# Performance work log

Measured on AMD Instinct MI355X. Metric: run time of the kernel, lower is better.

The kernel has to match this reference:

```python
import jax, jax.numpy as jnp
import numpy as np
from jax import lax

S = 1024   # max_num_segments
CB = 25    # color_hist_bins
TB = 10    # texture_hist_bins
EPS = 1e-12


def setup_inputs() -> dict:
    key = jax.random.key(0)
    k1, k2, k3, k4 = jax.random.split(key, 4)
    B, C, R, H, W = 8, 3, 8, 512, 512
    img = jax.random.normal(k1, (B, C, H, W), jnp.float32)
    imgs_bins = jax.random.randint(k2, (B, C, H, W), 0, CB, jnp.int32)
    grads_bins = jax.random.randint(k3, (B, C, R, H, W), 0, TB, jnp.int32)
    reg_lab = jax.random.randint(k4, (B, H, W), 0, S, jnp.int32)
    return {"img": img, "imgs_bins": imgs_bins, "grads_bins": grads_bins, "reg_lab": reg_lab}


def reference(img, imgs_bins, grads_bins, reg_lab):
    B, C, H, W = img.shape
    R = grads_bins.shape[2]
    HW = H * W
    lab = reg_lab.astype(jnp.int32)

    # ---- area_per_segment: scatter_add of ones over flattened labels ----
    flat = (lab.reshape(B, HW) + (jnp.arange(B, dtype=jnp.int32) * S)[:, None]).reshape(-1)
    area = jnp.zeros(B * S, jnp.int32).at[flat].add(1).reshape(B, S)

    # ---- bbox_per_segment: scatter amin/amax of pixel coordinates ----
    yy, xx = jnp.meshgrid(jnp.arange(H, dtype=jnp.int32),
                          jnp.arange(W, dtype=jnp.int32), indexing='ij')
    xb = jnp.broadcast_to(xx.reshape(HW), (B, HW)).reshape(-1)
    yb = jnp.broadcast_to(yy.reshape(HW), (B, HW)).reshape(-1)
    xmin = jnp.full(B * S, W, jnp.int32).at[flat].min(xb)
    ymin = jnp.full(B * S, H, jnp.int32).at[flat].min(yb)
    xmax = jnp.zeros(B * S, jnp.int32).at[flat].max(xb)
    ymax = jnp.zeros(B * S, jnp.int32).at[flat].max(yb)
    # torch does xywh[2:] -= xywh[:2] (no +1), so w = xmax - xmin
    bbox_xywh = jnp.stack([xmin, ymin, xmax - xmin, ymax - ymin], -1).reshape(B, S, 4)

    area_f = area.astype(jnp.float32)

    # ---- color histogram: scatter_add of ones into [B,C,S*CB] ----
    ci = (lab[:, None, :, :] * CB + imgs_bins).reshape(B * C, HW)
    ci = (ci + (jnp.arange(B * C, dtype=jnp.int32) * (S * CB))[:, None]).reshape(-1)
    color_hist = jnp.zeros(B * C * S * CB, jnp.float32).at[ci].add(1.0).reshape(B, C, S, CB)
    color_hist = color_hist.transpose(0, 2, 1, 3).reshape(B, S, C * CB)  # [B,S,C*CB]
    color_hist = color_hist / (area_f * float(C) + EPS)[..., None]

    # ---- texture histogram: scatter_add of ones into [B,C,R,S*TB] ----
    ti = (lab[:, None, None, :, :] * TB + grads_bins).reshape(B * C * R, HW)
    ti = (ti + (jnp.arange(B * C * R, dtype=jnp.int32) * (S * TB))[:, None]).reshape(-1)
    texture_hist = jnp.zeros(B * C * R * S * TB, jnp.float32).at[ti].add(1.0).reshape(B, C, R, S, TB)
    texture_hist = texture_hist.transpose(0, 3, 1, 2, 4).reshape(B, S, C * R * TB)  # [B,S,C*R*TB]
    texture_hist = texture_hist / (area_f * float(C * R) + EPS)[..., None]

    # ---- image_scharr_gradients: depthwise-style conv2d, padding=1 ----
    sx = jnp.array([[-3., 0., 3.], [-10., 0., 10.], [-3., 0., 3.]], jnp.float32)
    kern = jnp.stack([sx, sx.T])[:, None]  # [2,1,3,3]
    grads = lax.conv_general_dilated(img.reshape(B * C, 1, H, W), kern, (1, 1), 'SAME',
                                     dimension_numbers=('NCHW', 'OIHW', 'NCHW'))
    grads = grads.reshape(B, C, 2, H, W)

    return area, bbox_xywh, color_hist, texture_hist, grads
```

## Files before the change

### kernel.cpp

```cpp
#include <hip/hip_runtime.h>

#define B_ 8
#define C_ 3
#define R_ 8
#define H_ 512
#define W_ 512
#define HW_ (H_*W_)
#define S_ 1024
#define CB_ 25
#define TB_ 10

#define O_AREA 0
#define O_BBOX 8192
#define O_COLOR 40960
#define O_TEX 655360
#define O_GRADS 2621440
#define OUT_TOT 15204352

#define NTEX 192
#define NCOL 24
#define NBB  256
#define NHIST (NTEX + NCOL + NBB)
#define NCONV 768
#define NGRID1 (NHIST + NCONV)

#define SCR_WORDS (NBB * 2048)
#define NEED_WS ((size_t)SCR_WORDS * 4)
#define RID_ALL  786432
#define RID_SAFE 753664

__device__ __forceinline__ void conv_run(const float* __restrict__ img,
                                         float* __restrict__ out, int rid) {
  const int px0 = rid << 3;
  const int pix0 = px0 & (HW_ - 1);
  const int bc = px0 >> 18;
  const int x0 = pix0 & (W_ - 1);
  const int y = pix0 >> 9;
  const float* im = img + (size_t)bc * HW_ + pix0;
  const bool ym = y > 0, yp = y < H_ - 1, xm = x0 > 0, xp = x0 < W_ - 8;
  float r0[10], r1[10], r2[10];
  {
    const float4 a = *(const float4*)(im);
    const float4 c = *(const float4*)(im + 4);
    r1[1]=a.x; r1[2]=a.y; r1[3]=a.z; r1[4]=a.w;
    r1[5]=c.x; r1[6]=c.y; r1[7]=c.z; r1[8]=c.w;
    r1[0] = xm ? im[-1] : 0.f;  r1[9] = xp ? im[8] : 0.f;
  }
  if (ym) {
    const float* p = im - W_;
    const float4 a = *(const float4*)(p);
    const float4 c = *(const float4*)(p + 4);
    r0[1]=a.x; r0[2]=a.y; r0[3]=a.z; r0[4]=a.w;
    r0[5]=c.x; r0[6]=c.y; r0[7]=c.z; r0[8]=c.w;
    r0[0] = xm ? p[-1] : 0.f;  r0[9] = xp ? p[8] : 0.f;
  } else {
    #pragma unroll
    for (int i = 0; i < 10; ++i) r0[i] = 0.f;
  }
  if (yp) {
    const float* p = im + W_;
    const float4 a = *(const float4*)(p);
    const float4 c = *(const float4*)(p + 4);
    r2[1]=a.x; r2[2]=a.y; r2[3]=a.z; r2[4]=a.w;
    r2[5]=c.x; r2[6]=c.y; r2[7]=c.z; r2[8]=c.w;
    r2[0] = xm ? p[-1] : 0.f;  r2[9] = xp ? p[8] : 0.f;
  } else {
    #pragma unroll
    for (int i = 0; i < 10; ++i) r2[i] = 0.f;
  }
  float cs[10], dv[10];
  #pragma unroll
  for (int c = 0; c < 10; ++c) {
    cs[c] = 3.f * (r0[c] + r2[c]) + 10.f * r1[c];
    dv[c] = r2[c] - r0[c];
  }
  float gx[8], gy[8];
  #pragma unroll
  for (int k = 0; k < 8; ++k) {
    gx[k] = cs[k + 2] - cs[k];
    gy[k] = 3.f * (dv[k] + dv[k + 2]) + 10.f * dv[k + 1];
  }
  float* og = out + O_GRADS + (size_t)(bc * 2) * HW_ + pix0;
  *(float4*)(og)     = make_float4(gx[0], gx[1], gx[2], gx[3]);
  *(float4*)(og + 4) = make_float4(gx[4], gx[5], gx[6], gx[7]);
  float* oh = og + HW_;
  *(float4*)(oh)     = make_float4(gy[0], gy[1], gy[2], gy[3]);
  *(float4*)(oh + 4) = make_float4(gy[4], gy[5], gy[6], gy[7]);
}

__global__ __launch_bounds__(1024) void k_fused(
    const float* __restrict__ img,
    const int* __restrict__ imgs_bins,
    const int* __restrict__ grads_bins,
    const int* __restrict__ lab,
    float* __restrict__ out,
    unsigned* __restrict__ scr,
    int ridHi) {
  __shared__ unsigned smem[12800];
  const int bid = blockIdx.x;
  const int tid = threadIdx.x;

  if (bid >= NHIST) {
    const int rid = (bid - NHIST) * 1024 + tid;
    if (rid < ridHi) conv_run(img, out, rid);
  } else if (bid < NTEX) {
    const int plane = bid;
    const int b = plane / (C_*R_);
    const int cr = plane - b * (C_*R_);
    int* h = (int*)smem;
    for (int i = tid; i < S_*TB_; i += 1024) h[i] = 0;
    __syncthreads();
    const int4* bp = (const int4*)(grads_bins + (size_t)plane * HW_);
    const int4* lp = (const int4*)(lab + (size_t)b * HW_);
    int4 cb = bp[tid], cl = lp[tid];
    #pragma unroll 1
    for (int it = 1; it < 64; ++it) {
      const int4 nb = bp[it * 1024 + tid];
      const int4 nl = lp[it * 1024 + tid];
      atomicAdd(&h[cl.x*TB_ + cb.x], 1);
      atomicAdd(&h[cl.y*TB_ + cb.y], 1);
      atomicAdd(&h[cl.z*TB_ + cb.z], 1);
      atomicAdd(&h[cl.w*TB_ + cb.w], 1);
      cb = nb; cl = nl;
    }
    atomicAdd(&h[cl.x*TB_ + cb.x], 1);
    atomicAdd(&h[cl.y*TB_ + cb.y], 1);
    atomicAdd(&h[cl.z*TB_ + cb.z], 1);
    atomicAdd(&h[cl.w*TB_ + cb.w], 1);
    __syncthreads();
    {
      const int base = tid * TB_;
      int s = 0;
      #pragma unroll
      for (int t = 0; t < TB_; ++t) s += h[base + t];
      const float inv = 1.0f / ((float)s * 24.0f + 1e-12f);
      float* o = out + O_TEX + (size_t)b * (S_ * 240) + tid * 240 + cr * TB_;
      #pragma unroll
      for (int t = 0; t < TB_; ++t) o[t] = (float)h[base + t] * inv;
      if (cr == 0) out[O_AREA + b * S_ + tid] = (float)s;
    }
  } else if (bid < NTEX + NCOL) {
    const int plane = bid - NTEX;
    const int b = plane / C_;
    const int c = plane - b * C_;
    unsigned* h = smem;
    for (int i = tid; i < 12800; i += 1024) h[i] = 0;
    __syncthreads();
    const int4* bp = (const int4*)(imgs_bins + (size_t)plane * HW_);
    const int4* lp = (const int4*)(lab + (size_t)b * HW_);
    int4 cb = bp[tid], cl = lp[tid];
    #pragma unroll 1
    for (int it = 1; it < 64; ++it) {
      const int4 nb = bp[it * 1024 + tid];
      const int4 nl = lp[it * 1024 + tid];
      const int j0 = cl.x*CB_ + cb.x;
      const int j1 = cl.y*CB_ + cb.y;
      const int j2 = cl.z*CB_ + cb.z;
      const int j3 = cl.w*CB_ + cb.w;
      atomicAdd(&h[j0 >> 1], 1u << ((j0 & 1) << 4));
      atomicAdd(&h[j1 >> 1], 1u << ((j1 & 1) << 4));
      atomicAdd(&h[j2 >> 1], 1u << ((j2 & 1) << 4));
      atomicAdd(&h[j3 >> 1], 1u << ((j3 & 1) << 4));
      cb = nb; cl = nl;
    }
    {
      const int j0 = cl.x*CB_ + cb.x;
      const int j1 = cl.y*CB_ + cb.y;
      const int j2 = cl.z*CB_ + cb.z;
      const int j3 = cl.w*CB_ + cb.w;
      atomicAdd(&h[j0 >> 1], 1u << ((j0 & 1) << 4));
      atomicAdd(&h[j1 >> 1], 1u << ((j1 & 1) << 4));
      atomicAdd(&h[j2 >> 1], 1u << ((j2 & 1) << 4));
      atomicAdd(&h[j3 >> 1], 1u << ((j3 & 1) << 4));
    }
    __syncthreads();
    {
      int s = 0;
      #pragma unroll
      for (int ci = 0; ci < CB_; ++ci) {
        const int j = tid * CB_ + ci;
        s += (int)((h[j >> 1] >> ((j & 1) << 4)) & 0xFFFFu);
      }
      const float inv = 1.0f / ((float)s * 3.0f + 1e-12f);
      float* o = out + O_COLOR + (size_t)b * (S_ * 75) + tid * 75 + c * CB_;
      #pragma unroll
      for (int ci = 0; ci < CB_; ++ci) {
        const int j = tid * CB_ + ci;
        o[ci] = (float)((h[j >> 1] >> ((j & 1) << 4)) & 0xFFFFu) * inv;
      }
    }
  } else {
    const int rid2 = bid - NTEX - NCOL;
    const int b = rid2 >> 5, q = rid2 & 31;
    int* mn = (int*)smem;
    mn[tid] = W_; mn[1024 + tid] = H_; mn[2048 + tid] = 0; mn[3072 + tid] = 0;
    __syncthreads();
    const int4* lp = (const int4*)(lab + (size_t)b * HW_) + q * 2048;
    const int4 l0 = lp[tid], l1 = lp[tid + 1024];
    const int p0 = (q * 2048 + tid) * 4, p1 = p0 + 4096;
    #define BB(L,P) { const int yy = (P) >> 9, xx = (P) & (W_-1); \
      atomicMin(&mn[L], xx); atomicMin(&mn[1024 + (L)], yy); \
      atomicMax(&mn[2048 + (L)], xx); atomicMax(&mn[3072 + (L)], yy); }
    BB(l0.x, p0) BB(l0.y, p0+1) BB(l0.z, p0+2) BB(l0.w, p0+3)
    BB(l1.x, p1) BB(l1.y, p1+1) BB(l1.z, p1+2) BB(l1.w, p1+3)
    #undef BB
    __syncthreads();
    unsigned* dst = scr + (size_t)rid2 * 2048;
    dst[tid]        = (unsigned)mn[tid]        | ((unsigned)mn[1024 + tid] << 16);
    dst[1024 + tid] = (unsigned)mn[2048 + tid] | ((unsigned)mn[3072 + tid] << 16);
  }
}

__global__ __launch_bounds__(1024) void k_bb_merge(float* __restrict__ out,
                                                   const unsigned* __restrict__ scr) {
  const int b = blockIdx.x, l = threadIdx.x;
  int xmn = W_, ymn = H_, xmx = 0, ymx = 0;
  const unsigned* p = scr + (size_t)(b * 32) * 2048 + l;
  #pragma unroll
  for (int k = 0; k < 32; ++k) {
    const unsigned w0 = p[k * 2048];
    const unsigned w1 = p[k * 2048 + 1024];
    xmn = min(xmn, (int)(w0 & 0xFFFFu)); ymn = min(ymn, (int)(w0 >> 16));
    xmx = max(xmx, (int)(w1 & 0xFFFFu)); ymx = max(ymx, (int)(w1 >> 16));
  }
  float4 v;
  v.x = (float)xmn; v.y = (float)ymn;
  v.z = (float)(xmx - xmn); v.w = (float)(ymx - ymn);
  ((float4*)(out + O_BBOX))[b * S_ + l] = v;
}

__global__ __launch_bounds__(1024) void k_conv_tail(const float* __restrict__ img,
                                                    float* __restrict__ out) {
  conv_run(img, out, RID_SAFE + blockIdx.x * 1024 + threadIdx.x);
}

extern "C" void kernel_launch(void* const* d_in, const int* in_sizes, int n_in,
                              void* d_out, int out_size, void* d_ws, size_t ws_size,
                              hipStream_t stream) {
  const float* img = (const float*)d_in[0];
  const int* imgs_bins = (const int*)d_in[1];
  const int* grads_bins = (const int*)d_in[2];
  const int* reg_lab = (const int*)d_in[3];
  float* out = (float*)d_out;

  const bool ws_ok = ws_size >= NEED_WS;
  unsigned* scr = ws_ok ? (unsigned*)d_ws : (unsigned*)(out + (OUT_TOT - SCR_WORDS));
  const int ridHi = ws_ok ? RID_ALL : RID_SAFE;

  hipLaunchKernelGGL(k_fused, dim3(NGRID1), dim3(1024), 0, stream,
                     img, imgs_bins, grads_bins, reg_lab, out, scr, ridHi);
  hipLaunchKernelGGL(k_bb_merge, dim3(8), dim3(1024), 0, stream, out, scr);
  if (!ws_ok) {
    hipLaunchKernelGGL(k_conv_tail, dim3((RID_ALL - RID_SAFE) / 1024), dim3(1024),
                       0, stream, img, out);
  }
}
```

Baseline: 88.38 us.

## Merge bbox reduction into one block per batch and grid-stride conv blocks

Bounding-box computation now uses one block per batch image that loops over all pixels with shared-memory atomics and writes the final xywh directly. This removes the scratch buffer, the separate merge kernel and the fallback conv-tail kernel. Conv blocks are cut from 768 to 288 and use a grid-stride loop. The cost is 8 long-running bbox blocks doing 64 iterations of atomics each, which could become the critical path.

```diff
diff --git a/kernel.cpp b/kernel.cpp
--- a/kernel.cpp
+++ b/kernel.cpp
@@ -15,19 +15,15 @@
 #define O_COLOR 40960
 #define O_TEX 655360
 #define O_GRADS 2621440
-#define OUT_TOT 15204352
 
 #define NTEX 192
 #define NCOL 24
-#define NBB  256
+#define NBB  8
 #define NHIST (NTEX + NCOL + NBB)
-#define NCONV 768
-#define NGRID1 (NHIST + NCONV)
-
-#define SCR_WORDS (NBB * 2048)
-#define NEED_WS ((size_t)SCR_WORDS * 4)
-#define RID_ALL  786432
-#define RID_SAFE 753664
+#define NCONV 288
+#define NGRID (NHIST + NCONV)
+
+#define RID_ALL 786432
 
 __device__ __forceinline__ void conv_run(const float* __restrict__ img,
                                          float* __restrict__ out, int rid) {
@@ -93,16 +89,14 @@
     const int* __restrict__ imgs_bins,
     const int* __restrict__ grads_bins,
     const int* __restrict__ lab,
-    float* __restrict__ out,
-    unsigned* __restrict__ scr,
-    int ridHi) {
+    float* __restrict__ out) {
   __shared__ unsigned smem[12800];
   const int bid = blockIdx.x;
   const int tid = threadIdx.x;
 
   if (bid >= NHIST) {
-    const int rid = (bid - NHIST) * 1024 + tid;
-    if (rid < ridHi) conv_run(img, out, rid);
+    for (int rid = (bid - NHIST) * 1024 + tid; rid < RID_ALL; rid += NCONV * 1024)
+      conv_run(img, out, rid);
   } else if (bid < NTEX) {
     const int plane = bid;
     const int b = plane / (C_*R_);
@@ -190,48 +184,51 @@
       }
     }
   } else {
-    const int rid2 = bid - NTEX - NCOL;
-    const int b = rid2 >> 5, q = rid2 & 31;
+    const int b = bid - NTEX - NCOL;
     int* mn = (int*)smem;
     mn[tid] = W_; mn[1024 + tid] = H_; mn[2048 + tid] = 0; mn[3072 + tid] = 0;
     __syncthreads();
-    const int4* lp = (const int4*)(lab + (size_t)b * HW_) + q * 2048;
-    const int4 l0 = lp[tid], l1 = lp[tid + 1024];
-    const int p0 = (q * 2048 + tid) * 4, p1 = p0 + 4096;
-    #define BB(L,P) { const int yy = (P) >> 9, xx = (P) & (W_-1); \
-      atomicMin(&mn[L], xx); atomicMin(&mn[1024 + (L)], yy); \
-      atomicMax(&mn[2048 + (L)], xx); atomicMax(&mn[3072 + (L)], yy); }
-    BB(l0.x, p0) BB(l0.y, p0+1) BB(l0.z, p0+2) BB(l0.w, p0+3)
-    BB(l1.x, p1) BB(l1.y, p1+1) BB(l1.z, p1+2) BB(l1.w, p1+3)
-    #undef BB
-    __syncthreads();
-    unsigned* dst = scr + (size_t)rid2 * 2048;
-    dst[tid]        = (unsigned)mn[tid]        | ((unsigned)mn[1024 + tid] << 16);
-    dst[1024 + tid] = (unsigned)mn[2048 + tid] | ((unsigned)mn[3072 + tid] << 16);
-  }
-}
-
-__global__ __launch_bounds__(1024) void k_bb_merge(float* __restrict__ out,
-                                                   const unsigned* __restrict__ scr) {
-  const int b = blockIdx.x, l = threadIdx.x;
-  int xmn = W_, ymn = H_, xmx = 0, ymx = 0;
-  const unsigned* p = scr + (size_t)(b * 32) * 2048 + l;
-  #pragma unroll
-  for (int k = 0; k < 32; ++k) {
-    const unsigned w0 = p[k * 2048];
-    const unsigned w1 = p[k * 2048 + 1024];
-    xmn = min(xmn, (int)(w0 & 0xFFFFu)); ymn = min(ymn, (int)(w0 >> 16));
-    xmx = max(xmx, (int)(w1 & 0xFFFFu)); ymx = max(ymx, (int)(w1 >> 16));
-  }
-  float4 v;
-  v.x = (float)xmn; v.y = (float)ymn;
-  v.z = (float)(xmx - xmn); v.w = (float)(ymx - ymn);
-  ((float4*)(out + O_BBOX))[b * S_ + l] = v;
-}
-
-__global__ __launch_bounds__(1024) void k_conv_tail(const float* __restrict__ img,
-                                                    float* __restrict__ out) {
-  conv_run(img, out, RID_SAFE + blockIdx.x * 1024 + threadIdx.x);
+    const int4* lp = (const int4*)(lab + (size_t)b * HW_);
+    int4 cl = lp[tid];
+    #pragma unroll 1
+    for (int it = 1; it < 64; ++it) {
+      const int4 nl = lp[it * 1024 + tid];
+      const int p = ((it - 1) * 1024 + tid) * 4;
+      const int y = p >> 9;
+      const int x = p & (W_ - 1);
+      atomicMin(&mn[cl.x], x);       atomicMin(&mn[1024 + cl.x], y);
+      atomicMax(&mn[2048 + cl.x], x);     atomicMax(&mn[3072 + cl.x], y);
+      atomicMin(&mn[cl.y], x + 1);   atomicMin(&mn[1024 + cl.y], y);
+      atomicMax(&mn[2048 + cl.y], x + 1); atomicMax(&mn[3072 + cl.y], y);
+      atomicMin(&mn[cl.z], x + 2);   atomicMin(&mn[1024 + cl.z], y);
+      atomicMax(&mn[2048 + cl.z], x + 2); atomicMax(&mn[3072 + cl.z], y);
+      atomicMin(&mn[cl.w], x + 3);   atomicMin(&mn[1024 + cl.w], y);
+      atomicMax(&mn[2048 + cl.w], x + 3); atomicMax(&mn[3072 + cl.w], y);
+      cl = nl;
+    }
+    {
+      const int p = (63 * 1024 + tid) * 4;
+      const int y = p >> 9;
+      const int x = p & (W_ - 1);
+      atomicMin(&mn[cl.x], x);       atomicMin(&mn[1024 + cl.x], y);
+      atomicMax(&mn[2048 + cl.x], x);     atomicMax(&mn[3072 + cl.x], y);
+      atomicMin(&mn[cl.y], x + 1);   atomicMin(&mn[1024 + cl.y], y);
+      atomicMax(&mn[2048 + cl.y], x + 1); atomicMax(&mn[3072 + cl.y], y);
+      atomicMin(&mn[cl.z], x + 2);   atomicMin(&mn[1024 + cl.z], y);
+      atomicMax(&mn[2048 + cl.z], x + 2); atomicMax(&mn[3072 + cl.z], y);
+      atomicMin(&mn[cl.w], x + 3);   atomicMin(&mn[1024 + cl.w], y);
+      atomicMax(&mn[2048 + cl.w], x + 3); atomicMax(&mn[3072 + cl.w], y);
+    }
+    __syncthreads();
+    {
+      const int xmn = mn[tid], ymn = mn[1024 + tid];
+      const int xmx = mn[2048 + tid], ymx = mn[3072 + tid];
+      float4 v;
+      v.x = (float)xmn; v.y = (float)ymn;
+      v.z = (float)(xmx - xmn); v.w = (float)(ymx - ymn);
+      ((float4*)(out + O_BBOX))[b * S_ + tid] = v;
+    }
+  }
 }
 
 extern "C" void kernel_launch(void* const* d_in, const int* in_sizes, int n_in,
@@ -243,15 +240,6 @@
   const int* reg_lab = (const int*)d_in[3];
   float* out = (float*)d_out;
 
-  const bool ws_ok = ws_size >= NEED_WS;
-  unsigned* scr = ws_ok ? (unsigned*)d_ws : (unsigned*)(out + (OUT_TOT - SCR_WORDS));
-  const int ridHi = ws_ok ? RID_ALL : RID_SAFE;
-
-  hipLaunchKernelGGL(k_fused, dim3(NGRID1), dim3(1024), 0, stream,
-                     img, imgs_bins, grads_bins, reg_lab, out, scr, ridHi);
-  hipLaunchKernelGGL(k_bb_merge, dim3(8), dim3(1024), 0, stream, out, scr);
-  if (!ws_ok) {
-    hipLaunchKernelGGL(k_conv_tail, dim3((RID_ALL - RID_SAFE) / 1024), dim3(1024),
-                       0, stream, img, out);
-  }
+  hipLaunchKernelGGL(k_fused, dim3(NGRID), dim3(1024), 0, stream,
+                     img, imgs_bins, grads_bins, reg_lab, out);
 }
```

Measured after the change: 83.29 us. -5.8%, faster.
